# Optimization experiments

Hardware: AMD Instinct MI355X
Metric: run time of the kernel (lower is better)

The kernel has to match this reference:

```python
import jax, jax.numpy as jnp
import numpy as np


def setup_inputs() -> dict:
    key = jax.random.key(0)
    k1, k2, k3, k4 = jax.random.split(key, 4)
    B, T, E, H, D = 4, 2048, 1024, 16, 64
    x = jax.random.normal(k1, (B, T, E), dtype=jnp.float32)
    # wv stored as [E, H*D] so y = x @ wv (math-equivalent to nn.Linear weight.T)
    wv = jax.random.normal(k2, (E, H * D), dtype=jnp.float32) * (1.0 / E) ** 0.5
    wr = jax.random.normal(k3, (H, E, T), dtype=jnp.float32) * (2.0 / E) ** 0.5
    wo = jax.random.normal(k4, (H * D, E), dtype=jnp.float32) * (1.0 / (H * D)) ** 0.5
    return {"x": x, "wv": wv, "wr": wr, "wo": wo}


def reference(x, wv, wr, wo):
    B, T, E = x.shape
    H = wr.shape[0]
    HD = wv.shape[1]
    D = HD // H
    # values: [B, H, T, D]
    v = (x @ wv).reshape(B, T, H, D).transpose(0, 2, 1, 3)
    # per-key scores, identical for every query row: s[b,h,k]
    s = jnp.einsum('bte,het->bht', x, wr[:, :, :T]) / jnp.sqrt(jnp.asarray(D, x.dtype))
    # causal softmax over keys k<=q with scores shared across queries reduces to
    # a prefix-softmax-weighted cumulative sum over V (exact same math, O(T)):
    # out[q] = sum_{k<=q} exp(s_k - m) v_k / sum_{k<=q} exp(s_k - m)
    m = jnp.max(s, axis=-1, keepdims=True)          # global max is a valid stable shift
    e = jnp.exp(s - m)                              # [B,H,T]
    num = jnp.cumsum(e[..., None] * v, axis=2)      # [B,H,T,D]
    den = jnp.cumsum(e, axis=2)[..., None]          # [B,H,T,1]
    out = num / den                                 # [B,H,T,D]
    out = out.transpose(0, 2, 1, 3).reshape(B, T, HD)
    return out @ wo
```

## Files before the change

### kernel.cpp

```cpp
#include <hip/hip_runtime.h>
#include <stdint.h>

typedef unsigned short u16;
typedef __attribute__((ext_vector_type(8))) short short8;
typedef __attribute__((ext_vector_type(8))) unsigned short ushort8v;
typedef __attribute__((ext_vector_type(4))) float f32x4;

#define B_  4
#define T_  2048
#define E_  1024
#define H_  16
#define D_  64
#define HD_ 1024
#define BT_ (B_*T_)
#define TC_ 64
#define NC_ (T_/TC_)
#define SG_ 32
#define SEB_ (E_/SG_)
#define SHB_ 2

__device__ __forceinline__ u16 f2b(float f) {
  uint32_t u = __float_as_uint(f);
  uint32_t r = (u + 0x7FFFu + ((u >> 16) & 1u)) >> 16;
  return (u16)r;
}
__device__ __forceinline__ float b2f(u16 u) {
  return __uint_as_float(((uint32_t)u) << 16);
}

__global__ __launch_bounds__(256) void prep_all(const float* __restrict__ x,
                                                const float* __restrict__ wv,
                                                const float* __restrict__ wo,
                                                u16* __restrict__ xb,
                                                u16* __restrict__ xTb8,
                                                u16* __restrict__ wvT,
                                                u16* __restrict__ woT) {
  __shared__ float tile[64][65];
  const int bid = blockIdx.x;
  if (bid < 2048) {
    const int b = bid >> 9, rest = bid & 511;
    const int t0 = (rest >> 4) * 64, e0 = (rest & 15) * 64;
    const int c4 = (threadIdx.x & 15) * 4;
    const int rw = threadIdx.x >> 4;
#pragma unroll
    for (int r = 0; r < 4; ++r) {
      const int row = r * 16 + rw;
      const float4 v4 = *reinterpret_cast<const float4*>(
          &x[((size_t)b * T_ + t0 + row) * E_ + e0 + c4]);
      tile[row][c4 + 0] = v4.x; tile[row][c4 + 1] = v4.y;
      tile[row][c4 + 2] = v4.z; tile[row][c4 + 3] = v4.w;
      ushort4 o;
      o.x = f2b(v4.x); o.y = f2b(v4.y); o.z = f2b(v4.z); o.w = f2b(v4.w);
      *reinterpret_cast<ushort4*>(&xb[((size_t)(b * T_ + t0 + row)) * E_ + e0 + c4]) = o;
    }
    __syncthreads();
    const int tl = threadIdx.x & 63;
    const int eg = threadIdx.x >> 6;
#pragma unroll
    for (int p = 0; p < 2; ++p) {
      const int egg = eg + p * 4;
      ushort8v o;
#pragma unroll
      for (int j = 0; j < 8; ++j) o[j] = f2b(tile[tl][egg * 8 + j]);
      *reinterpret_cast<ushort8v*>(
          &xTb8[((size_t)(b * (E_ / 8) + (e0 >> 3) + egg) * T_ + t0 + tl) * 8]) = o;
    }
  } else {
    const int k = bid - 2048;
    const float* in = (k >> 8) ? wo : wv;
    u16* out = (k >> 8) ? woT : wvT;
    const int r0 = ((k >> 4) & 15) * 64, c0 = (k & 15) * 64;
    const int tx = threadIdx.x & 63, ty = threadIdx.x >> 6;
#pragma unroll
    for (int r = 0; r < 16; ++r) {
      int row = r * 4 + ty;
      tile[row][tx] = in[(size_t)(r0 + row) * 1024 + c0 + tx];
    }
    __syncthreads();
#pragma unroll
    for (int r = 0; r < 16; ++r) {
      int row = r * 4 + ty;
      out[(size_t)(c0 + row) * 1024 + r0 + tx] = f2b(tile[tx][row]);
    }
  }
}

template <int OUT_BF16>
__global__ __launch_bounds__(256) void gemm_bt(const u16* __restrict__ A,
                                               const u16* __restrict__ Bt,
                                               float* __restrict__ Cf,
                                               u16* __restrict__ Cb,
                                               int M, int N, int K) {
  __shared__ __align__(16) u16 As[128 * 64];
  __shared__ __align__(16) u16 Bs[128 * 64];
  const int tid  = threadIdx.x;
  const int lane = tid & 63;
  const int wave = tid >> 6;
  const int wr_  = wave >> 1, wc_ = wave & 1;

  const int nwg = gridDim.x * gridDim.y;
  const int bid = blockIdx.y * gridDim.x + blockIdx.x;
  const int cpx = nwg >> 3;
  const int swz = (bid & 7) * cpx + (bid >> 3);
  const int bx = swz % gridDim.x, by = swz / gridDim.x;
  const int brow = by * 128;
  const int bcol = bx * 128;
  const int l15 = lane & 15, l4 = lane >> 4;

  f32x4 acc[4][4];
  const f32x4 zero = {0.f, 0.f, 0.f, 0.f};
#pragma unroll
  for (int i = 0; i < 4; ++i)
#pragma unroll
    for (int j = 0; j < 4; ++j) acc[i][j] = zero;

  for (int k0 = 0; k0 < K; k0 += 64) {
#pragma unroll
    for (int s2 = 0; s2 < 4; ++s2) {
      const int c = s2 * 256 + tid;
      const int row = c >> 3, g = c & 7;
      const int gs = g ^ (row & 7);
      const u16* ga = A  + (size_t)(brow + row) * K + k0 + gs * 8;
      const u16* gb = Bt + (size_t)(bcol + row) * K + k0 + gs * 8;
      u16* la = &As[(size_t)(s2 * 256 + wave * 64) * 8];
      u16* lb = &Bs[(size_t)(s2 * 256 + wave * 64) * 8];
      __builtin_amdgcn_global_load_lds((const __attribute__((address_space(1))) void*)ga,
                                       (__attribute__((address_space(3))) void*)la,
                                       16, 0, 0);
      __builtin_amdgcn_global_load_lds((const __attribute__((address_space(1))) void*)gb,
                                       (__attribute__((address_space(3))) void*)lb,
                                       16, 0, 0);
    }
    __syncthreads();

    short8 af[2][4], bfr[2][4];
#pragma unroll
    for (int kk = 0; kk < 2; ++kk) {
      const int sg = (kk * 4 + l4) ^ (l15 & 7);
#pragma unroll
      for (int mi = 0; mi < 4; ++mi)
        af[kk][mi] = *reinterpret_cast<const short8*>(
            &As[(wr_ * 64 + mi * 16 + l15) * 64 + sg * 8]);
#pragma unroll
      for (int ni = 0; ni < 4; ++ni)
        bfr[kk][ni] = *reinterpret_cast<const short8*>(
            &Bs[(wc_ * 64 + ni * 16 + l15) * 64 + sg * 8]);
    }
#pragma unroll
    for (int kk = 0; kk < 2; ++kk)
#pragma unroll
      for (int mi = 0; mi < 4; ++mi)
#pragma unroll
        for (int ni = 0; ni < 4; ++ni)
          acc[mi][ni] = __builtin_amdgcn_mfma_f32_16x16x32_bf16(af[kk][mi], bfr[kk][ni],
                                                                acc[mi][ni], 0, 0, 0);
    __syncthreads();
  }

#pragma unroll
  for (int mi = 0; mi < 4; ++mi) {
#pragma unroll
    for (int ni = 0; ni < 4; ++ni) {
      const int col = bcol + wc_ * 64 + ni * 16 + l15;
#pragma unroll
      for (int j = 0; j < 4; ++j) {
        const int row = brow + wr_ * 64 + mi * 16 + l4 * 4 + j;
        if (OUT_BF16) Cb[(size_t)row * N + col] = f2b(acc[mi][ni][j]);
        else          Cf[(size_t)row * N + col] = acc[mi][ni][j];
      }
    }
  }
}

__global__ __launch_bounds__(256) void score_partial(const u16* __restrict__ xTb8,
                                                     const float* __restrict__ wr,
                                                     u16* __restrict__ partial) {
  const int t  = blockIdx.x * 256 + threadIdx.x;
  const int g  = blockIdx.y;
  const int h0 = blockIdx.z * SHB_;
  float acc[4][SHB_];
#pragma unroll
  for (int b = 0; b < 4; ++b)
#pragma unroll
    for (int hh = 0; hh < SHB_; ++hh) acc[b][hh] = 0.f;

#pragma unroll
  for (int e8 = 0; e8 < SEB_ / 8; ++e8) {
    const int eb = g * (SEB_ / 8) + e8;
    ushort8v xv[4];
#pragma unroll
    for (int b = 0; b < 4; ++b)
      xv[b] = *reinterpret_cast<const ushort8v*>(
          &xTb8[((size_t)(b * (E_ / 8) + eb) * T_ + t) * 8]);
#pragma unroll
    for (int j = 0; j < 8; ++j) {
      const int e = eb * 8 + j;
      float xf[4];
#pragma unroll
      for (int b = 0; b < 4; ++b) xf[b] = b2f(xv[b][j]);
#pragma unroll
      for (int hh = 0; hh < SHB_; ++hh) {
        const float w = wr[((size_t)(h0 + hh) * E_ + e) * T_ + t];
#pragma unroll
        for (int b = 0; b < 4; ++b) acc[b][hh] = fmaf(xf[b], w, acc[b][hh]);
      }
    }
  }
  u16* pp = partial + (size_t)g * (B_ * H_ * T_);
#pragma unroll
  for (int b = 0; b < 4; ++b)
#pragma unroll
    for (int hh = 0; hh < SHB_; ++hh)
      pp[((size_t)b * H_ + h0 + hh) * T_ + t] = f2b(acc[b][hh] * 0.125f);
}

__global__ __launch_bounds__(256) void chunk_sums(const u16* __restrict__ partial,
                                                  const u16* __restrict__ v,
                                                  float* __restrict__ s,
                                                  float* __restrict__ sev,
                                                  float* __restrict__ se,
                                                  float* __restrict__ mc) {
  const int bh = blockIdx.y;
  const int b = bh >> 4, h = bh & 15;
  const int w = threadIdx.x >> 6, d = threadIdx.x & 63;
  const int c = blockIdx.x * 4 + w;
  const int t = blockIdx.x * 256 + threadIdx.x;

  float sv = 0.f;
#pragma unroll
  for (int g = 0; g < SG_; ++g)
    sv += b2f(partial[(size_t)g * (B_ * H_ * T_) + (size_t)bh * T_ + t]);
  s[(size_t)bh * T_ + t] = sv;

  __shared__ float es[4][64];
  es[w][d] = sv;

  float lm = sv;
#pragma unroll
  for (int off = 1; off < 64; off <<= 1) lm = fmaxf(lm, __shfl_xor(lm, off, 64));

  const u16* vp = v + ((size_t)(b * T_ + c * TC_)) * HD_ + h * D_ + d;
  float acc = 0.f, ae = 0.f;
#pragma unroll 8
  for (int tt = 0; tt < TC_; ++tt) {
    float e = __expf(es[w][tt] - lm);
    acc = fmaf(e, b2f(vp[(size_t)tt * HD_]), acc);
    ae += e;
  }
  sev[((size_t)bh * NC_ + c) * D_ + d] = acc;
  if (d == 0) { se[bh * NC_ + c] = ae; mc[bh * NC_ + c] = lm; }
}

__global__ __launch_bounds__(256) void chunk_scan(const float* __restrict__ s,
                                                  const u16* __restrict__ v,
                                                  const float* __restrict__ sev,
                                                  const float* __restrict__ se,
                                                  const float* __restrict__ mc,
                                                  u16* __restrict__ attn) {
  const int bh = blockIdx.y;
  const int b = bh >> 4, h = bh & 15;
  const int w = threadIdx.x >> 6, d = threadIdx.x & 63;
  const int c = blockIdx.x * 4 + w;
  const float* mcp = mc + bh * NC_;

  float gm = (d < NC_) ? mcp[d] : -1e30f;
#pragma unroll
  for (int off = 1; off < 64; off <<= 1) gm = fmaxf(gm, __shfl_xor(gm, off, 64));

  const float* sevp = sev + (size_t)bh * NC_ * D_;
  const float* sep  = se + bh * NC_;
  float pn = 0.f, pd = 0.f;
  for (int c2 = 0; c2 < c; ++c2) {
    float f = __expf(mcp[c2] - gm);
    pn = fmaf(sevp[(size_t)c2 * D_ + d], f, pn);
    pd = fmaf(sep[c2], f, pd);
  }

  const float* sp = s + (size_t)bh * T_ + c * TC_;
  const u16* vp = v + ((size_t)(b * T_ + c * TC_)) * HD_ + h * D_ + d;
  u16* ap = attn + ((size_t)(b * T_ + c * TC_)) * HD_ + h * D_ + d;
#pragma unroll 8
  for (int tt = 0; tt < TC_; ++tt) {
    float e = __expf(sp[tt] - gm);
    pn = fmaf(e, b2f(vp[(size_t)tt * HD_]), pn);
    pd += e;
    ap[(size_t)tt * HD_] = f2b(__fdividef(pn, pd));
  }
}

extern "C" void kernel_launch(void* const* d_in, const int* in_sizes, int n_in,
                              void* d_out, int out_size, void* d_ws, size_t ws_size,
                              hipStream_t stream) {
  const float* x  = (const float*)d_in[0];
  const float* wv = (const float*)d_in[1];
  const float* wr = (const float*)d_in[2];
  const float* wo = (const float*)d_in[3];
  float* out = (float*)d_out;

  char* ws = (char*)d_ws;
  size_t off = 0;
  auto alloc = [&](size_t bytes) {
    void* p = ws + off;
    off += (bytes + 255) & ~(size_t)255;
    return p;
  };
  u16*   xb   = (u16*)  alloc((size_t)BT_ * E_ * 2);
  u16*   xTb8 = (u16*)  alloc((size_t)B_ * E_ * T_ * 2);
  u16*   wvT  = (u16*)  alloc((size_t)HD_ * E_ * 2);
  u16*   woT  = (u16*)  alloc((size_t)E_ * HD_ * 2);
  u16*   vv   = (u16*)  alloc((size_t)BT_ * HD_ * 2);
  u16*   attn = (u16*)  alloc((size_t)BT_ * HD_ * 2);
  float* s    = (float*)alloc((size_t)B_ * H_ * T_ * 4);
  float* sev  = (float*)alloc((size_t)B_ * H_ * NC_ * D_ * 4);
  float* se   = (float*)alloc((size_t)B_ * H_ * NC_ * 4);
  float* mc   = (float*)alloc((size_t)B_ * H_ * NC_ * 4);
  u16*   part = (u16*)  alloc((size_t)SG_ * B_ * H_ * T_ * 2);

  prep_all<<<2560, 256, 0, stream>>>(x, wv, wo, xb, xTb8, wvT, woT);

  gemm_bt<1><<<dim3(HD_ / 128, BT_ / 128), 256, 0, stream>>>(xb, wvT, nullptr, vv, BT_, HD_, E_);

  score_partial<<<dim3(T_ / 256, SG_, H_ / SHB_), 256, 0, stream>>>(xTb8, wr, part);

  chunk_sums<<<dim3(NC_ / 4, B_ * H_), 256, 0, stream>>>(part, vv, s, sev, se, mc);
  chunk_scan<<<dim3(NC_ / 4, B_ * H_), 256, 0, stream>>>(s, vv, sev, se, mc, attn);

  gemm_bt<0><<<dim3(E_ / 128, BT_ / 128), 256, 0, stream>>>(attn, woT, out, nullptr, BT_, E_, HD_);
}
```

Before: 121.8 us.

## Multi-stage LDS pipeline with async prefetch in the bf16 GEMM

Rewrites the GEMM main loop from a single-buffered 64-wide K tile into a 4-slot ring buffer of 32-wide K tiles. Loads run three stages ahead and each step waits on an explicit vmcnt count, so there is one barrier per step instead of two. The swizzle is adjusted for the narrower tile, and the MFMA block is wrapped in a raised wave priority. The aim is to hide global-to-LDS latency behind the matrix math, at the cost of twice the LDS per block, which may lower occupancy.

```diff
diff --git a/kernel.cpp b/kernel.cpp
--- a/kernel.cpp
+++ b/kernel.cpp
@@ -91,8 +91,8 @@
                                                float* __restrict__ Cf,
                                                u16* __restrict__ Cb,
                                                int M, int N, int K) {
-  __shared__ __align__(16) u16 As[128 * 64];
-  __shared__ __align__(16) u16 Bs[128 * 64];
+  __shared__ __align__(16) u16 As[4][128 * 32];
+  __shared__ __align__(16) u16 Bs[4][128 * 32];
   const int tid  = threadIdx.x;
   const int lane = tid & 63;
   const int wave = tid >> 6;
@@ -114,16 +114,18 @@
 #pragma unroll
     for (int j = 0; j < 4; ++j) acc[i][j] = zero;
 
-  for (int k0 = 0; k0 < K; k0 += 64) {
-#pragma unroll
-    for (int s2 = 0; s2 < 4; ++s2) {
+  auto stage = [&](int kt) {
+    const int k0 = kt * 32;
+    const int slot = kt & 3;
+#pragma unroll
+    for (int s2 = 0; s2 < 2; ++s2) {
       const int c = s2 * 256 + tid;
-      const int row = c >> 3, g = c & 7;
-      const int gs = g ^ (row & 7);
+      const int row = c >> 2, g = c & 3;
+      const int gs = g ^ ((row >> 1) & 3);
       const u16* ga = A  + (size_t)(brow + row) * K + k0 + gs * 8;
       const u16* gb = Bt + (size_t)(bcol + row) * K + k0 + gs * 8;
-      u16* la = &As[(size_t)(s2 * 256 + wave * 64) * 8];
-      u16* lb = &Bs[(size_t)(s2 * 256 + wave * 64) * 8];
+      u16* la = &As[slot][(size_t)(s2 * 256 + wave * 64) * 8];
+      u16* lb = &Bs[slot][(size_t)(s2 * 256 + wave * 64) * 8];
       __builtin_amdgcn_global_load_lds((const __attribute__((address_space(1))) void*)ga,
                                        (__attribute__((address_space(3))) void*)la,
                                        16, 0, 0);
@@ -131,31 +133,45 @@
                                        (__attribute__((address_space(3))) void*)lb,
                                        16, 0, 0);
     }
-    __syncthreads();
-
-    short8 af[2][4], bfr[2][4];
-#pragma unroll
-    for (int kk = 0; kk < 2; ++kk) {
-      const int sg = (kk * 4 + l4) ^ (l15 & 7);
-#pragma unroll
-      for (int mi = 0; mi < 4; ++mi)
-        af[kk][mi] = *reinterpret_cast<const short8*>(
-            &As[(wr_ * 64 + mi * 16 + l15) * 64 + sg * 8]);
-#pragma unroll
-      for (int ni = 0; ni < 4; ++ni)
-        bfr[kk][ni] = *reinterpret_cast<const short8*>(
-            &Bs[(wc_ * 64 + ni * 16 + l15) * 64 + sg * 8]);
-    }
-#pragma unroll
-    for (int kk = 0; kk < 2; ++kk)
-#pragma unroll
-      for (int mi = 0; mi < 4; ++mi)
-#pragma unroll
-        for (int ni = 0; ni < 4; ++ni)
-          acc[mi][ni] = __builtin_amdgcn_mfma_f32_16x16x32_bf16(af[kk][mi], bfr[kk][ni],
-                                                                acc[mi][ni], 0, 0, 0);
-    __syncthreads();
-  }
+  };
+
+  const int sgr = l4 ^ ((l15 >> 1) & 3);
+
+#define GSTEP(KT, VMC, DOSTAGE)                                               \
+  do {                                                                        \
+    asm volatile("s_waitcnt vmcnt(" #VMC ")" ::: "memory");                   \
+    __builtin_amdgcn_s_barrier();                                             \
+    __builtin_amdgcn_sched_barrier(0);                                        \
+    if (DOSTAGE) stage((KT) + 3);                                             \
+    const int slot_ = (KT) & 3;                                               \
+    short8 af[4], bf[4];                                                      \
+    _Pragma("unroll")                                                         \
+    for (int mi = 0; mi < 4; ++mi)                                            \
+      af[mi] = *reinterpret_cast<const short8*>(                              \
+          &As[slot_][((wr_ * 64 + mi * 16 + l15) * 4 + sgr) * 8]);            \
+    _Pragma("unroll")                                                         \
+    for (int ni = 0; ni < 4; ++ni)                                            \
+      bf[ni] = *reinterpret_cast<const short8*>(                              \
+          &Bs[slot_][((wc_ * 64 + ni * 16 + l15) * 4 + sgr) * 8]);            \
+    __builtin_amdgcn_s_setprio(1);                                            \
+    _Pragma("unroll")                                                         \
+    for (int mi = 0; mi < 4; ++mi)                                            \
+      _Pragma("unroll")                                                       \
+      for (int ni = 0; ni < 4; ++ni)                                          \
+        acc[mi][ni] = __builtin_amdgcn_mfma_f32_16x16x32_bf16(                \
+            af[mi], bf[ni], acc[mi][ni], 0, 0, 0);                            \
+    __builtin_amdgcn_s_setprio(0);                                            \
+  } while (0)
+
+  const int NK = K / 32;
+  stage(0); stage(1); stage(2);
+
+  for (int kt = 0; kt < NK - 2; ++kt) {
+    GSTEP(kt, 8, kt + 3 < NK);
+  }
+  GSTEP(NK - 2, 4, false);
+  GSTEP(NK - 1, 0, false);
+#undef GSTEP
 
 #pragma unroll
   for (int mi = 0; mi < 4; ++mi) {
```

Result: slower. 125.3 us (+2.8%).
